# Optimization experiments

Hardware: AMD Instinct MI355X
Metric: run time of the kernel (lower is better)

The kernel has to match this reference:

```python
import jax, jax.numpy as jnp
import numpy as np
import math

B, SEQ, PRED, F, DM, NH, DFF, S, DMARK = 16, 336, 96, 7, 512, 8, 2048, 16, 5
EL, DL = 2, 1
DH = DM // NH


def _pe(max_len, d):
    pos = np.arange(max_len)[:, None].astype(np.float32)
    div = np.exp(np.arange(0, d, 2).astype(np.float32) * (-math.log(10000.0) / d))
    pe = np.zeros((max_len, d), np.float32)
    pe[:, 0::2] = np.sin(pos * div)
    pe[:, 1::2] = np.cos(pos * div)
    return jnp.asarray(pe)


def _make_tao():
    t = np.ones((S, S), np.float32)
    t[:, 0] = 0.0
    t[:, -1] = 0.0
    t[1] *= -1.0
    t[0] = 0.0
    t[0, 0] = 1.0
    t[2:, 1:-1] = np.eye(S - 2, dtype=np.float32)
    return jnp.asarray(t)


PE = _pe(2000, DM)
TAO = _make_tao()
ZVEC = jnp.zeros((S,), jnp.float32).at[:2].set(1.0)
MASK = jnp.triu(jnp.full((PRED, PRED), -1e9, jnp.float32), k=1)  # causal additive mask


def _ln(x, w, b, eps=1e-5):
    m = x.mean(-1, keepdims=True)
    v = ((x - m) ** 2).mean(-1, keepdims=True)
    return (x - m) * jax.lax.rsqrt(v + eps) * w + b


def _mha(q_in, kv_in, qkv_w, qkv_b, ow, ob, mask=None):
    wq, wk, wv = jnp.split(qkv_w, 3, axis=0)
    bq, bk, bv = jnp.split(qkv_b, 3, axis=0)

    def proj(x, w, bb):
        y = x @ w.T + bb  # [B, T, DM]
        return y.reshape(y.shape[0], y.shape[1], NH, DH).transpose(0, 2, 1, 3)

    q, k, v = proj(q_in, wq, bq), proj(kv_in, wk, bk), proj(kv_in, wv, bv)
    s = jnp.einsum('bhqd,bhkd->bhqk', q, k) / math.sqrt(DH)
    if mask is not None:
        s = s + mask
    a = jax.nn.softmax(s, axis=-1)
    o = jnp.einsum('bhqk,bhkd->bhqd', a, v)
    o = o.transpose(0, 2, 1, 3).reshape(q_in.shape)
    return o @ ow.T + ob


def _per_feature(xe, xd, eqw, eqb, eow, eob, el1w, el1b, el2w, el2b,
                 ef1w, ef1b, ef2w, ef2b, elw, elb,
                 dsqw, dsqb, dsow, dsob, dcqw, dcqb, dcow, dcob,
                 dl1w, dl1b, dl2w, dl2b, dl3w, dl3b, df1w, df1b, df2w, df2b):
    # post-norm TransformerEncoder (relu FFN), eval mode (no dropout)
    h = xe
    for l in range(EL):
        h = _ln(h + _mha(h, h, eqw[l], eqb[l], eow[l], eob[l]), el1w[l], el1b[l])
        ff = jax.nn.relu(h @ ef1w[l].T + ef1b[l]) @ ef2w[l].T + ef2b[l]
        h = _ln(h + ff, el2w[l], el2b[l])
    # encoder_linear maps time axis seqlen -> prelen
    mem = jnp.einsum('bsd,ps->bpd', h, elw) + elb[None, :, None]
    t = xd
    for l in range(DL):
        t = _ln(t + _mha(t, t, dsqw[l], dsqb[l], dsow[l], dsob[l], MASK), dl1w[l], dl1b[l])
        t = _ln(t + _mha(t, mem, dcqw[l], dcqb[l], dcow[l], dcob[l]), dl2w[l], dl2b[l])
        ff = jax.nn.relu(t @ df1w[l].T + df1b[l]) @ df2w[l].T + df2b[l]
        t = _ln(t + ff, dl3w[l], dl3b[l])
    return t


_vfeat = jax.vmap(_per_feature, in_axes=(1, 1) + (0,) * 32, out_axes=1)


def setup_inputs():
    key = jax.random.key(0)
    ks = iter(jax.random.split(key, 64))

    def rn(shape, s=0.05):
        return jax.random.normal(next(ks), shape, jnp.float32) * s

    return {
        'batch_x': rn((B, SEQ, F), 1.0),
        'batch_x_mark': rn((B, SEQ, DMARK - 1), 1.0),
        'batch_y': rn((B, PRED, F), 1.0),
        'batch_y_mark': rn((B, PRED, DMARK - 1), 1.0),
        'w_in': rn((DM, DMARK)), 'b_in': rn((DM,)),
        'w_co': rn((DM, DMARK - 1)), 'b_co': rn((DM,)),
        'eqw': rn((F, EL, 3 * DM, DM)), 'eqb': rn((F, EL, 3 * DM)),
        'eow': rn((F, EL, DM, DM)), 'eob': rn((F, EL, DM)),
        'el1w': jnp.ones((F, EL, DM)), 'el1b': jnp.zeros((F, EL, DM)),
        'el2w': jnp.ones((F, EL, DM)), 'el2b': jnp.zeros((F, EL, DM)),
        'ef1w': rn((F, EL, DFF, DM)), 'ef1b': rn((F, EL, DFF)),
        'ef2w': rn((F, EL, DM, DFF)), 'ef2b': rn((F, EL, DM)),
        'elw': rn((F, PRED, SEQ)), 'elb': rn((F, PRED)),
        'dsqw': rn((F, DL, 3 * DM, DM)), 'dsqb': rn((F, DL, 3 * DM)),
        'dsow': rn((F, DL, DM, DM)), 'dsob': rn((F, DL, DM)),
        'dcqw': rn((F, DL, 3 * DM, DM)), 'dcqb': rn((F, DL, 3 * DM)),
        'dcow': rn((F, DL, DM, DM)), 'dcob': rn((F, DL, DM)),
        'dl1w': jnp.ones((F, DL, DM)), 'dl1b': jnp.zeros((F, DL, DM)),
        'dl2w': jnp.ones((F, DL, DM)), 'dl2b': jnp.zeros((F, DL, DM)),
        'dl3w': jnp.ones((F, DL, DM)), 'dl3b': jnp.zeros((F, DL, DM)),
        'df1w': rn((F, DL, DFF, DM)), 'df1b': rn((F, DL, DFF)),
        'df2w': rn((F, DL, DM, DFF)), 'df2b': rn((F, DL, DM)),
        'wc': rn((S, DM)), 'bc': rn((S,)),
        'ws': rn((1, DM)), 'bs': rn((1,)),
    }


def reference(batch_x, batch_x_mark, batch_y, batch_y_mark,
              w_in, b_in, w_co, b_co,
              eqw, eqb, eow, eob, el1w, el1b, el2w, el2b,
              ef1w, ef1b, ef2w, ef2b, elw, elb,
              dsqw, dsqb, dsow, dsob, dcqw, dcqb, dcow, dcob,
              dl1w, dl1b, dl2w, dl2b, dl3w, dl3b, df1w, df1b, df2w, df2b,
              wc, bc, ws, bs):
    Bsz = batch_x.shape[0]
    # time marks are shared across features -> broadcast instead of concat loop
    hist = jnp.concatenate(
        [batch_x[..., None],
         jnp.broadcast_to(batch_x_mark[:, :, None, :], (Bsz, SEQ, F, DMARK - 1))], axis=-1)
    fut = jnp.broadcast_to(batch_y_mark[:, -PRED:, None, :], (Bsz, PRED, F, DMARK - 1))
    hist = hist.transpose(0, 2, 1, 3)  # [B, F, SEQ, DMARK]
    fut = fut.transpose(0, 2, 1, 3)    # [B, F, PRED, DMARK-1]
    xe = hist @ w_in.T + b_in + PE[:SEQ]
    xd = fut @ w_co.T + b_co + PE[:PRED]
    dec = _vfeat(xe, xd, eqw, eqb, eow, eob, el1w, el1b, el2w, el2b,
                 ef1w, ef1b, ef2w, ef2b, elw, elb,
                 dsqw, dsqb, dsow, dsob, dcqw, dcqb, dcow, dcob,
                 dl1w, dl1b, dl2w, dl2b, dl3w, dl3b, df1w, df1b, df2w, df2b)
    # g_c = Linear + Hardsigmoid; g_s = Linear + Softplus
    c = jnp.clip((jnp.einsum('bfpd,sd->bfps', dec, wc) + bc) / 6.0 + 0.5, 0.0, 1.0)
    sig = jax.nn.softplus(jnp.einsum('bfpd,d->bfp', dec, ws[0]) + bs[0])
    # linear state recurrence a = TAO @ a + c, y = z^T a, scanned over prediction days
    a0 = c[:, :, 0]                      # [B, F, S] (torch initializes a with day-0 g_c)
    cs = jnp.moveaxis(c, 2, 0)           # [PRED, B, F, S]
    ss = jnp.moveaxis(sig, 2, 0)         # [PRED, B, F]

    def step(a, xs):
        cd, sd = xs
        a = jnp.einsum('ij,bfj->bfi', TAO, a) + cd
        return a, jnp.einsum('s,bfs->bf', ZVEC, a) + sd

    _, ys = jax.lax.scan(step, a0, (cs, ss))
    return jnp.transpose(ys, (1, 0, 2))  # [B, PRED, F]
```

## Files before the change

### kernel.cpp

```cpp
#include <hip/hip_runtime.h>

typedef unsigned short u16;
typedef unsigned int   u32;
typedef __attribute__((ext_vector_type(8))) short short8;
typedef __attribute__((ext_vector_type(4))) float f32x4;

#define DEV static __device__ __forceinline__

DEV float bf2f(u16 u) { return __uint_as_float(((u32)u) << 16); }
DEV u16 f2bf(float f) {
  u32 u = __float_as_uint(f);
  return (u16)((u + 0x7fffu + ((u >> 16) & 1u)) >> 16);
}

#define GLD16(gp, lp) __builtin_amdgcn_global_load_lds( \
    (__attribute__((address_space(1))) u32*)(gp),       \
    (__attribute__((address_space(3))) u32*)(lp), 16, 0, 0)

__global__ __launch_bounds__(512, 2) void gemm_bf16(
    const u16* __restrict__ A, const u16* __restrict__ Bw, u16* __restrict__ C,
    const float* __restrict__ bias, int M, int N, int K,
    long sAz, long sBz, long sCz, long sBiasZ, int relu)
{
  __shared__ __align__(16) u16 Asm[2][256 * 64];
  __shared__ __align__(16) u16 Bsm[2][256 * 64];

  int gx = (int)gridDim.x, gy = (int)gridDim.y;
  int nwg = gx * gy * (int)gridDim.z;
  int orig = (int)blockIdx.x + gx * ((int)blockIdx.y + gy * (int)blockIdx.z);
  int q = nwg >> 3, r = nwg & 7;
  int xcd = orig & 7, pos = orig >> 3;
  int lg_id = (xcd < r) ? (xcd * (q + 1) + pos) : (r * (q + 1) + (xcd - r) * q + pos);
  int bz = lg_id / (gx * gy);
  int rem = lg_id - bz * (gx * gy);
  int by = rem / gx, bx = rem - by * gx;

  A += (size_t)bz * sAz; Bw += (size_t)bz * sBz; C += (size_t)bz * sCz; bias += (size_t)bz * sBiasZ;
  int tileM = bx * 256, tileN = by * 256;
  int tid = threadIdx.x, wave = tid >> 6, lane = tid & 63;
  int lr = lane & 15, lgp = lane >> 4;
  int wm = (wave >> 2) * 128;
  int wn = (wave & 3) * 64;

  const int NT = K >> 6;

  auto STAGE = [&](int b, int t) {
    int kb = t * 64;
    #pragma unroll
    for (int i = 0; i < 4; i++) {
      int gi = i * 512 + wave * 64 + lane;
      int row = gi >> 3, g = gi & 7;
      int gsw = (g ^ (row & 7)) * 8;
      GLD16(A + (size_t)(tileM + row) * K + kb + gsw, &Asm[b][(size_t)gi * 8]);
      GLD16(Bw + (size_t)(tileN + row) * K + kb + gsw, &Bsm[b][(size_t)gi * 8]);
    }
  };

  f32x4 acc[8][4] = {};

  STAGE(0, 0);
  if (NT > 1) STAGE(1, 1);

  for (int t = 0; t < NT; ++t) {
    int cur = t & 1;
    if (t + 1 < NT) asm volatile("s_waitcnt vmcnt(8)" ::: "memory");
    else            asm volatile("s_waitcnt vmcnt(0)" ::: "memory");
    asm volatile("s_barrier" ::: "memory");

    const u16* Ab = Asm[cur];
    const u16* Bb = Bsm[cur];
    #pragma unroll
    for (int ks = 0; ks < 2; ++ks) {
      short8 bfr[4], afr[8];
      #pragma unroll
      for (int n = 0; n < 4; ++n) {
        int row = wn + n * 16 + lr;
        bfr[n] = *(const short8*)(Bb + row * 64 + (((ks * 4 + lgp) ^ (row & 7)) * 8));
      }
      #pragma unroll
      for (int m = 0; m < 8; ++m) {
        int row = wm + m * 16 + lr;
        afr[m] = *(const short8*)(Ab + row * 64 + (((ks * 4 + lgp) ^ (row & 7)) * 8));
      }
      __builtin_amdgcn_s_setprio(1);
      #pragma unroll
      for (int m = 0; m < 8; ++m)
        #pragma unroll
        for (int n = 0; n < 4; ++n)
          acc[m][n] = __builtin_amdgcn_mfma_f32_16x16x32_bf16(afr[m], bfr[n], acc[m][n], 0, 0, 0);
      __builtin_amdgcn_s_setprio(0);
    }
    asm volatile("s_waitcnt lgkmcnt(0)" ::: "memory");
    asm volatile("s_barrier" ::: "memory");
    if (t + 2 < NT) STAGE(cur, t + 2);
  }

  float bb[4];
  #pragma unroll
  for (int n = 0; n < 4; ++n) bb[n] = bias[tileN + wn + n * 16 + lr];
  #pragma unroll
  for (int m = 0; m < 8; ++m) {
    #pragma unroll
    for (int rr = 0; rr < 4; ++rr) {
      int mrow = tileM + wm + m * 16 + lgp * 4 + rr;
      u16* crow = C + (size_t)mrow * N + tileN + wn + lr;
      #pragma unroll
      for (int n = 0; n < 4; ++n) {
        float v = acc[m][n][rr] + bb[n];
        if (relu) v = fmaxf(v, 0.f);
        crow[n * 16] = f2bf(v);
      }
    }
  }
}

__global__ void cvt_w_kernel(const float* __restrict__ src, u16* __restrict__ dst,
                             long n_per_f, long f_stride, long total4)
{
  long i = (long)blockIdx.x * blockDim.x + threadIdx.x;
  long step = (long)gridDim.x * blockDim.x;
  for (; i < total4; i += step) {
    long e = i * 4;
    long f = e / n_per_f; long r = e - f * n_per_f;
    float4 v = *(const float4*)(src + f * f_stride + r);
    *(ushort4*)(dst + e) = make_ushort4(f2bf(v.x), f2bf(v.y), f2bf(v.z), f2bf(v.w));
  }
}

__global__ __launch_bounds__(128) void embed_enc_k(
    const float* __restrict__ x, const float* __restrict__ mark,
    const float* __restrict__ w_in, const float* __restrict__ b_in,
    u16* __restrict__ hb)
{
  int row = blockIdx.x;
  int f = row / 5376; int rem = row - f * 5376; int b = rem / 336; int s = rem - b * 336;
  int bsix = b * 336 + s;
  float v0 = x[(size_t)bsix * 7 + f];
  float m0 = mark[(size_t)bsix * 4 + 0], m1 = mark[(size_t)bsix * 4 + 1];
  float m2 = mark[(size_t)bsix * 4 + 2], m3 = mark[(size_t)bsix * 4 + 3];
  int d0 = threadIdx.x * 4;
  u16 ob[4];
  #pragma unroll
  for (int c = 0; c < 4; c++) {
    int d = d0 + c;
    const float* w = w_in + d * 5;
    float val = w[0] * v0 + w[1] * m0 + w[2] * m1 + w[3] * m2 + w[4] * m3 + b_in[d];
    int i = d >> 1;
    float dv = expf((float)i * -0.0359778920778f);
    float arg = (float)s * dv;
    val += (d & 1) ? cosf(arg) : sinf(arg);
    ob[c] = f2bf(val);
  }
  *(ushort4*)(hb + (size_t)row * 512 + d0) = make_ushort4(ob[0], ob[1], ob[2], ob[3]);
}

__global__ __launch_bounds__(128) void embed_dec_k(
    const float* __restrict__ ymark, const float* __restrict__ w_co,
    const float* __restrict__ b_co, u16* __restrict__ tb)
{
  int row = blockIdx.x;
  int f = row / 1536; int rem = row - f * 1536; int b = rem / 96; int pp = rem - b * 96;
  int bp = b * 96 + pp;
  float m0 = ymark[(size_t)bp * 4 + 0], m1 = ymark[(size_t)bp * 4 + 1];
  float m2 = ymark[(size_t)bp * 4 + 2], m3 = ymark[(size_t)bp * 4 + 3];
  int d0 = threadIdx.x * 4;
  u16 ob[4];
  #pragma unroll
  for (int c = 0; c < 4; c++) {
    int d = d0 + c;
    const float* w = w_co + d * 4;
    float val = w[0] * m0 + w[1] * m1 + w[2] * m2 + w[3] * m3 + b_co[d];
    int i = d >> 1;
    float dv = expf((float)i * -0.0359778920778f);
    float arg = (float)pp * dv;
    val += (d & 1) ? cosf(arg) : sinf(arg);
    ob[c] = f2bf(val);
  }
  *(ushort4*)(tb + (size_t)row * 512 + d0) = make_ushort4(ob[0], ob[1], ob[2], ob[3]);
}

template<int LK, int CHUNK, int NQI>
__global__ __launch_bounds__(256) void attn_mfma(
    const u16* __restrict__ q, const u16* __restrict__ k, const u16* __restrict__ v,
    u16* __restrict__ out, int Lq, int qstride, int kvstride, int causal, int qspan)
{
  constexpr int NCH = LK / CHUNK;
  constexpr int NKT = CHUNK / 16;
  constexpr int NKS = (CHUNK + 31) / 32;
  constexpr int KPAD = NKS * 32;
  constexpr int VSTR = KPAD + 8;
  constexpr int NGRP = CHUNK * 8 / 64;

  __shared__ __align__(16) u16 KsS[CHUNK * 64];
  __shared__ __align__(16) u16 VtS[64 * VSTR];
  __shared__ __align__(16) u16 PWS[4][16 * VSTR];

  int hh = blockIdx.x, fb = blockIdx.y;
  int tid = threadIdx.x, wave = tid >> 6, lane = tid & 63;
  int lr = lane & 15, lg = lane >> 4;

  const int nqt = Lq / 16;
  const int qlo = (int)blockIdx.z * qspan;
  const int qhi = (qlo + qspan < nqt) ? (qlo + qspan) : nqt;

  const u16* qp = q + (size_t)fb * Lq * qstride + hh * 64;
  const u16* kp = k + (size_t)fb * LK * kvstride + hh * 64;
  const u16* vp = v + (size_t)fb * LK * kvstride + hh * 64;

  if constexpr (KPAD > CHUNK) {
    constexpr int TW = KPAD - CHUNK;
    for (int i = tid; i < 64 * TW; i += 256)
      VtS[(i / TW) * VSTR + CHUNK + (i % TW)] = 0;
    u16* PW = PWS[wave];
    for (int i = lane; i < 16 * TW; i += 64)
      PW[(i / TW) * VSTR + CHUNK + (i % TW)] = 0;
  }

  f32x4 oacc[NQI][4] = {};
  f32x4 lsum[NQI] = {};
  u16* PW = PWS[wave];

  for (int c = 0; c < NCH; ++c) {
    __syncthreads();

    const u16* kcp = kp + (size_t)c * CHUNK * kvstride;
    for (int grp = wave; grp < NGRP; grp += 4) {
      int gi = grp * 64 + lane;
      int row = gi >> 3, g = gi & 7;
      GLD16(kcp + (size_t)row * kvstride + ((g ^ (row & 7)) * 8), KsS + (size_t)gi * 8);
    }
    const u16* vcp = vp + (size_t)c * CHUNK * kvstride;
    for (int idx = tid; idx < CHUNK * 8; idx += 256) {
      int kk = idx >> 3, dg = idx & 7;
      uint4 pv = *(const uint4*)(vcp + (size_t)kk * kvstride + dg * 8);
      u16* col = VtS + (size_t)(dg * 8) * VSTR + kk;
      col[0 * VSTR] = (u16)pv.x; col[1 * VSTR] = (u16)(pv.x >> 16);
      col[2 * VSTR] = (u16)pv.y; col[3 * VSTR] = (u16)(pv.y >> 16);
      col[4 * VSTR] = (u16)pv.z; col[5 * VSTR] = (u16)(pv.z >> 16);
      col[6 * VSTR] = (u16)pv.w; col[7 * VSTR] = (u16)(pv.w >> 16);
    }
    __syncthreads();

    #pragma unroll
    for (int qi = 0; qi < NQI; ++qi) {
      int qt = qlo + wave + qi * 4;
      if (qt < qhi) {
        const u16* qrow = qp + (size_t)(qt * 16 + lr) * qstride + lg * 8;
        short8 qf0 = *(const short8*)(qrow);
        short8 qf1 = *(const short8*)(qrow + 32);

        f32x4 sacc[NKT];
        #pragma unroll
        for (int t = 0; t < NKT; t++) {
          int row = t * 16 + lr;
          const u16* kb = KsS + row * 64;
          short8 kf0 = *(const short8*)(kb + ((lg ^ (row & 7)) * 8));
          short8 kf1 = *(const short8*)(kb + (((lg + 4) ^ (row & 7)) * 8));
          f32x4 s = {0.f, 0.f, 0.f, 0.f};
          s = __builtin_amdgcn_mfma_f32_16x16x32_bf16(qf0, kf0, s, 0, 0, 0);
          s = __builtin_amdgcn_mfma_f32_16x16x32_bf16(qf1, kf1, s, 0, 0, 0);
          sacc[t] = s;
        }

        #pragma unroll
        for (int t = 0; t < NKT; t++) {
          int kg = c * CHUNK + t * 16 + lr;
          #pragma unroll
          for (int r = 0; r < 4; r++) {
            int qg = qt * 16 + lg * 4 + r;
            float p = (causal && kg > qg) ? 0.f : __expf(sacc[t][r] * 0.125f);
            sacc[t][r] = p;
            lsum[qi][r] += p;
          }
          u16* pw = PW + (size_t)(lg * 4) * VSTR + t * 16 + lr;
          pw[0 * VSTR] = f2bf(sacc[t][0]);
          pw[1 * VSTR] = f2bf(sacc[t][1]);
          pw[2 * VSTR] = f2bf(sacc[t][2]);
          pw[3 * VSTR] = f2bf(sacc[t][3]);
        }

        #pragma unroll
        for (int s = 0; s < NKS; s++) {
          short8 pf = *(const short8*)(PW + (size_t)lr * VSTR + s * 32 + lg * 8);
          #pragma unroll
          for (int j = 0; j < 4; j++) {
            short8 vf = *(const short8*)(VtS + (size_t)(j * 16 + lr) * VSTR + s * 32 + lg * 8);
            oacc[qi][j] = __builtin_amdgcn_mfma_f32_16x16x32_bf16(pf, vf, oacc[qi][j], 0, 0, 0);
          }
        }
      }
    }
  }

  #pragma unroll
  for (int qi = 0; qi < NQI; ++qi) {
    int qt = qlo + wave + qi * 4;
    if (qt < qhi) {
      float l0 = lsum[qi][0], l1 = lsum[qi][1], l2 = lsum[qi][2], l3 = lsum[qi][3];
      #pragma unroll
      for (int m = 1; m < 16; m <<= 1) {
        l0 += __shfl_xor(l0, m);
        l1 += __shfl_xor(l1, m);
        l2 += __shfl_xor(l2, m);
        l3 += __shfl_xor(l3, m);
      }
      float inv[4] = {1.f / l0, 1.f / l1, 1.f / l2, 1.f / l3};
      #pragma unroll
      for (int r = 0; r < 4; r++) {
        size_t orow = (size_t)fb * Lq + qt * 16 + lg * 4 + r;
        u16* ob = out + orow * 512 + hh * 64 + lr;
        #pragma unroll
        for (int j = 0; j < 4; j++)
          ob[j * 16] = f2bf(oacc[qi][j][r] * inv[r]);
      }
    }
  }
}

__global__ __launch_bounds__(128) void ln_kernel(
    u16* __restrict__ h, const u16* __restrict__ delta,
    const float* __restrict__ gamma, const float* __restrict__ beta,
    int rows_per_f, long gstride)
{
  __shared__ float red[2];
  int row = blockIdx.x;
  int f = row / rows_per_f;
  const float* g = gamma + (size_t)f * gstride;
  const float* be = beta + (size_t)f * gstride;
  int d0 = threadIdx.x * 4;
  size_t p = (size_t)row * 512 + d0;
  ushort4 hv = *(const ushort4*)(h + p);
  ushort4 dv = *(const ushort4*)(delta + p);
  float x0 = bf2f(hv.x) + bf2f(dv.x), x1 = bf2f(hv.y) + bf2f(dv.y);
  float x2 = bf2f(hv.z) + bf2f(dv.z), x3 = bf2f(hv.w) + bf2f(dv.w);
  float ssum = x0 + x1 + x2 + x3;
  #pragma unroll
  for (int m = 1; m < 64; m <<= 1) ssum += __shfl_xor(ssum, m);
  if ((threadIdx.x & 63) == 0) red[threadIdx.x >> 6] = ssum;
  __syncthreads();
  float mean = (red[0] + red[1]) * (1.f / 512.f);
  __syncthreads();
  float c0 = x0 - mean, c1 = x1 - mean, c2 = x2 - mean, c3 = x3 - mean;
  float sq = c0 * c0 + c1 * c1 + c2 * c2 + c3 * c3;
  #pragma unroll
  for (int m = 1; m < 64; m <<= 1) sq += __shfl_xor(sq, m);
  if ((threadIdx.x & 63) == 0) red[threadIdx.x >> 6] = sq;
  __syncthreads();
  float var = (red[0] + red[1]) * (1.f / 512.f);
  float rstd = rsqrtf(var + 1e-5f);
  float y0 = c0 * rstd * g[d0 + 0] + be[d0 + 0];
  float y1 = c1 * rstd * g[d0 + 1] + be[d0 + 1];
  float y2 = c2 * rstd * g[d0 + 2] + be[d0 + 2];
  float y3 = c3 * rstd * g[d0 + 3] + be[d0 + 3];
  *(ushort4*)(h + p) = make_ushort4(f2bf(y0), f2bf(y1), f2bf(y2), f2bf(y3));
}

__global__ __launch_bounds__(256) void mem_kernel(
    const u16* __restrict__ h, const float* __restrict__ elw,
    const float* __restrict__ elb, u16* __restrict__ memb)
{
  int fb = blockIdx.x; int f = fb >> 4;
  int pc = blockIdx.y;
  int d0 = threadIdx.x * 2;
  const u16* hbase = h + (size_t)fb * 336 * 512;
  const float* wbase = elw + (size_t)f * 96 * 336 + (size_t)pc * 16 * 336;
  float a0[16], a1[16];
  #pragma unroll
  for (int pp = 0; pp < 16; pp++) { a0[pp] = 0.f; a1[pp] = 0.f; }
  for (int s = 0; s < 336; s++) {
    ushort2 h2 = *(const ushort2*)(hbase + (size_t)s * 512 + d0);
    float hx = bf2f(h2.x), hy = bf2f(h2.y);
    #pragma unroll
    for (int pp = 0; pp < 16; pp++) {
      float w = wbase[pp * 336 + s];
      a0[pp] += w * hx; a1[pp] += w * hy;
    }
  }
  #pragma unroll
  for (int pp = 0; pp < 16; pp++) {
    int pidx = pc * 16 + pp;
    size_t row = (size_t)fb * 96 + pidx;
    float e = elb[f * 96 + pidx];
    *(ushort2*)(memb + row * 512 + d0) = make_ushort2(f2bf(a0[pp] + e), f2bf(a1[pp] + e));
  }
}

__global__ __launch_bounds__(64) void head_kernel(
    const u16* __restrict__ td, const float* __restrict__ wcp, const float* __restrict__ bcp,
    const float* __restrict__ wsp, const float* __restrict__ bsp,
    float* __restrict__ cb, float* __restrict__ sg, int f0)
{
  int rl = blockIdx.x, lane = threadIdx.x;
  size_t row = (size_t)f0 * 1536 + rl;
  const u16* x = td + (size_t)rl * 512;
  float xr[8];
  #pragma unroll
  for (int j = 0; j < 8; j++) xr[j] = bf2f(x[lane + 64 * j]);
  #pragma unroll
  for (int o = 0; o < 16; o++) {
    const float* w = wcp + o * 512;
    float p = 0.f;
    #pragma unroll
    for (int j = 0; j < 8; j++) p += xr[j] * w[lane + 64 * j];
    #pragma unroll
    for (int m = 1; m < 64; m <<= 1) p += __shfl_xor(p, m);
    if (lane == 0) {
      float cv = (p + bcp[o]) / 6.0f + 0.5f;
      cb[row * 16 + o] = fminf(fmaxf(cv, 0.f), 1.f);
    }
  }
  float p = 0.f;
  #pragma unroll
  for (int j = 0; j < 8; j++) p += xr[j] * wsp[lane + 64 * j];
  #pragma unroll
  for (int m = 1; m < 64; m <<= 1) p += __shfl_xor(p, m);
  if (lane == 0) {
    float zv = p + bsp[0];
    sg[row] = (zv > 20.f) ? zv : log1pf(expf(zv));
  }
}

__global__ __launch_bounds__(256) void scan_kernel(
    const float* __restrict__ cbuf, const float* __restrict__ sgb, float* __restrict__ outp)
{
  int f = blockIdx.x;
  int b = threadIdx.x >> 4;
  int s = threadIdx.x & 15;
  size_t rbase = ((size_t)f * 16 + b) * 96;
  float a = cbuf[rbase * 16 + s];
  for (int p = 0; p < 96; ++p) {
    float cd = cbuf[(rbase + p) * 16 + s];
    float sd = sgb[rbase + p];
    float xs = (s >= 1 && s <= 14) ? a : 0.f;
    #pragma unroll
    for (int m = 1; m < 16; m <<= 1) xs += __shfl_xor(xs, m);
    float up = __shfl_up(a, 1, 16);
    float an = (s == 0) ? (a + cd) : ((s == 1) ? (cd - xs) : (up + cd));
    a = an;
    float y01 = __shfl(a, 0, 16) + __shfl(a, 1, 16) + sd;
    if (s == 0) outp[((size_t)b * 96 + p) * 7 + f] = y01;
  }
}

__global__ void diag_kernel(float* __restrict__ out, float v, int n)
{
  int i = blockIdx.x * 256 + threadIdx.x;
  if (i < n) out[i] = v;
}

extern "C" void kernel_launch(void* const* d_in, const int* in_sizes, int n_in,
                              void* d_out, int out_size, void* d_ws, size_t ws_size,
                              hipStream_t stream)
{
  (void)in_sizes; (void)n_in;
  const float* batch_x      = (const float*)d_in[0];
  const float* batch_x_mark = (const float*)d_in[1];
  const float* batch_y_mark = (const float*)d_in[3];
  const float* w_in = (const float*)d_in[4];
  const float* b_in = (const float*)d_in[5];
  const float* w_co = (const float*)d_in[6];
  const float* b_co = (const float*)d_in[7];
  const float* eqw  = (const float*)d_in[8];
  const float* eqb  = (const float*)d_in[9];
  const float* eow  = (const float*)d_in[10];
  const float* eob  = (const float*)d_in[11];
  const float* el1w = (const float*)d_in[12];
  const float* el1b = (const float*)d_in[13];
  const float* el2w = (const float*)d_in[14];
  const float* el2b = (const float*)d_in[15];
  const float* ef1w = (const float*)d_in[16];
  const float* ef1b = (const float*)d_in[17];
  const float* ef2w = (const float*)d_in[18];
  const float* ef2b = (const float*)d_in[19];
  const float* elw  = (const float*)d_in[20];
  const float* elb  = (const float*)d_in[21];
  const float* dsqw = (const float*)d_in[22];
  const float* dsqb = (const float*)d_in[23];
  const float* dsow = (const float*)d_in[24];
  const float* dsob = (const float*)d_in[25];
  const float* dcqw = (const float*)d_in[26];
  const float* dcqb = (const float*)d_in[27];
  const float* dcow = (const float*)d_in[28];
  const float* dcob = (const float*)d_in[29];
  const float* dl1w = (const float*)d_in[30];
  const float* dl1b = (const float*)d_in[31];
  const float* dl2w = (const float*)d_in[32];
  const float* dl2b = (const float*)d_in[33];
  const float* dl3w = (const float*)d_in[34];
  const float* dl3b = (const float*)d_in[35];
  const float* df1w = (const float*)d_in[36];
  const float* df1b = (const float*)d_in[37];
  const float* df2w = (const float*)d_in[38];
  const float* df2b = (const float*)d_in[39];
  const float* wc   = (const float*)d_in[40];
  const float* bc   = (const float*)d_in[41];
  const float* wsg  = (const float*)d_in[42];
  const float* bsg  = (const float*)d_in[43];

  const size_t NE = 37632;
  const size_t ND = 10752;
  auto al = [](size_t x) { return (x + 255) & ~(size_t)255; };

  size_t fixedB = al(NE * 1024) + al(ND * 1024) + al(ND * 64) + al(ND * 4);
  int G = 0;
  for (int g = 7; g >= 1; --g) {
    size_t need = fixedB
        + al((size_t)g * 5376 * 2048 * 2)
        + al((size_t)g * 5376 * 512 * 2)
        + al((size_t)g * 2048 * 512 * 2)
        + al((size_t)g * 1536 * 512 * 2);
    if (need <= ws_size) { G = g; break; }
  }
  if (G == 0) {
    diag_kernel<<<dim3((out_size + 255) / 256), 256, 0, stream>>>(
        (float*)d_out, 1000.0f + (float)(ws_size >> 20), out_size);
    return;
  }

  char* base = (char*)d_ws;
  size_t off = 0;
  auto alloc = [&](size_t bytes) -> void* { void* r = base + off; off += al(bytes); return r; };
  u16*   hres = (u16*)  alloc(NE * 1024);
  u16*   tres = (u16*)  alloc(ND * 1024);
  float* cb   = (float*)alloc(ND * 64);
  float* sg   = (float*)alloc(ND * 4);
  u16*   bigc = (u16*)  alloc((size_t)G * 5376 * 2048 * 2);
  u16*   aobc = (u16*)  alloc((size_t)G * 5376 * 512 * 2);
  u16*   wbuf = (u16*)  alloc((size_t)G * 2048 * 512 * 2);
  u16*   memb = (u16*)  alloc((size_t)G * 1536 * 512 * 2);

  embed_enc_k<<<dim3(37632), 128, 0, stream>>>(batch_x, batch_x_mark, w_in, b_in, hres);
  embed_dec_k<<<dim3(10752), 128, 0, stream>>>(batch_y_mark, w_co, b_co, tres);

  auto cvtw = [&](const float* src, long n_per_f, long f_stride, int g) {
    cvt_w_kernel<<<dim3(512), 256, 0, stream>>>(src, wbuf, n_per_f, f_stride,
                                                (long)g * n_per_f / 4);
  };
  auto gemm = [&](const u16* A, long sAz, u16* C, long sCz, const float* bias, long sBias,
                  int M, int N, int K, int g, int relu) {
    dim3 gr(M / 256, N / 256, g);
    gemm_bf16<<<gr, 512, 0, stream>>>(A, wbuf, C, bias, M, N, K, sAz, (long)N * K, sCz,
                                      sBias, relu);
  };

  for (int f0 = 0; f0 < 7; f0 += G) {
    int g = (7 - f0 < G) ? (7 - f0) : G;
    u16* hc = hres + (size_t)f0 * 5376 * 512;
    u16* tc = tres + (size_t)f0 * 1536 * 512;

    for (int l = 0; l < 2; ++l) {
      cvtw(eqw + (size_t)f0 * 1572864 + (size_t)l * 786432, 786432L, 1572864L, g);
      gemm(hc, 5376L * 512, bigc, 5376L * 1536, eqb + f0 * 3072 + l * 1536, 3072,
           5376, 1536, 512, g, 0);
      attn_mfma<336, 112, 3><<<dim3(8, g * 16, 2), 256, 0, stream>>>(
          bigc, bigc + 512, bigc + 1024, aobc, 336, 1536, 1536, 0, 11);
      cvtw(eow + (size_t)f0 * 524288 + (size_t)l * 262144, 262144L, 524288L, g);
      gemm(aobc, 5376L * 512, bigc, 5376L * 512, eob + f0 * 1024 + l * 512, 1024,
           5376, 512, 512, g, 0);
      ln_kernel<<<dim3(g * 5376), 128, 0, stream>>>(
          hc, bigc, el1w + f0 * 1024 + l * 512, el1b + f0 * 1024 + l * 512, 5376, 1024);
      cvtw(ef1w + (size_t)f0 * 2097152 + (size_t)l * 1048576, 1048576L, 2097152L, g);
      gemm(hc, 5376L * 512, bigc, 5376L * 2048, ef1b + f0 * 4096 + l * 2048, 4096,
           5376, 2048, 512, g, 1);
      cvtw(ef2w + (size_t)f0 * 2097152 + (size_t)l * 1048576, 1048576L, 2097152L, g);
      gemm(bigc, 5376L * 2048, aobc, 5376L * 512, ef2b + f0 * 1024 + l * 512, 1024,
           5376, 512, 2048, g, 0);
      ln_kernel<<<dim3(g * 5376), 128, 0, stream>>>(
          hc, aobc, el2w + f0 * 1024 + l * 512, el2b + f0 * 1024 + l * 512, 5376, 1024);
    }

    mem_kernel<<<dim3(g * 16, 6), 256, 0, stream>>>(
        hc, elw + (size_t)f0 * 32256, elb + f0 * 96, memb);

    cvtw(dsqw + (size_t)f0 * 786432, 786432L, 786432L, g);
    gemm(tc, 1536L * 512, bigc, 1536L * 1536, dsqb + f0 * 1536, 1536,
         1536, 1536, 512, g, 0);
    attn_mfma<96, 96, 2><<<dim3(8, g * 16, 1), 256, 0, stream>>>(
        bigc, bigc + 512, bigc + 1024, aobc, 96, 1536, 1536, 1, 6);
    cvtw(dsow + (size_t)f0 * 262144, 262144L, 262144L, g);
    gemm(aobc, 1536L * 512, bigc, 1536L * 512, dsob + f0 * 512, 512,
         1536, 512, 512, g, 0);
    ln_kernel<<<dim3(g * 1536), 128, 0, stream>>>(
        tc, bigc, dl1w + f0 * 512, dl1b + f0 * 512, 1536, 512);

    cvtw(dcqw + (size_t)f0 * 786432, 262144L, 786432L, g);
    gemm(tc, 1536L * 512, bigc, 1536L * 512, dcqb + f0 * 1536, 1536,
         1536, 512, 512, g, 0);
    u16* bigKV = bigc + (size_t)g * 1536 * 512;
    cvtw(dcqw + (size_t)f0 * 786432 + 262144, 524288L, 786432L, g);
    gemm(memb, 1536L * 512, bigKV, 1536L * 1024, dcqb + f0 * 1536 + 512, 1536,
         1536, 1024, 512, g, 0);
    attn_mfma<96, 96, 2><<<dim3(8, g * 16, 1), 256, 0, stream>>>(
        bigc, bigKV, bigKV + 512, aobc, 96, 512, 1024, 0, 6);
    cvtw(dcow + (size_t)f0 * 262144, 262144L, 262144L, g);
    gemm(aobc, 1536L * 512, bigc, 1536L * 512, dcob + f0 * 512, 512,
         1536, 512, 512, g, 0);
    ln_kernel<<<dim3(g * 1536), 128, 0, stream>>>(
        tc, bigc, dl2w + f0 * 512, dl2b + f0 * 512, 1536, 512);

    cvtw(df1w + (size_t)f0 * 1048576, 1048576L, 1048576L, g);
    gemm(tc, 1536L * 512, bigc, 1536L * 2048, df1b + f0 * 2048, 2048,
         1536, 2048, 512, g, 1);
    cvtw(df2w + (size_t)f0 * 1048576, 1048576L, 1048576L, g);
    gemm(bigc, 1536L * 2048, aobc, 1536L * 512, df2b + f0 * 512, 512,
         1536, 512, 2048, g, 0);
    ln_kernel<<<dim3(g * 1536), 128, 0, stream>>>(
        tc, aobc, dl3w + f0 * 512, dl3b + f0 * 512, 1536, 512);

    head_kernel<<<dim3(g * 1536), 64, 0, stream>>>(tc, wc, bc, wsg, bsg, cb, sg, f0);
  }

  scan_kernel<<<dim3(7), 256, 0, stream>>>(cb, sg, (float*)d_out);
}
```

Measured before the change: 1.578 ms.

## Restructure GEMM main loop into four-phase ping-pong with split half-tile staging

The bf16 GEMM main loop now splits the A and B shared-memory tiles into two halves each. Each K-step is broken into four MFMA quadrants, with LDS fragment reads and global-to-LDS loads of the next halves interleaved between barriers. The goal is to overlap global loads and LDS reads with matrix-core work instead of staging whole tiles after the compute. It adds more barriers and depends on careful vmcnt accounting, which could cause stalls or hazards if the counts are wrong.

```diff
diff --git a/kernel.cpp b/kernel.cpp
--- a/kernel.cpp
+++ b/kernel.cpp
@@ -17,20 +17,23 @@
     (__attribute__((address_space(1))) u32*)(gp),       \
     (__attribute__((address_space(3))) u32*)(lp), 16, 0, 0)
 
+#define SBAR()  asm volatile("s_barrier" ::: "memory")
+#define LGKM0() asm volatile("s_waitcnt lgkmcnt(0)" ::: "memory")
+
 __global__ __launch_bounds__(512, 2) void gemm_bf16(
     const u16* __restrict__ A, const u16* __restrict__ Bw, u16* __restrict__ C,
     const float* __restrict__ bias, int M, int N, int K,
     long sAz, long sBz, long sCz, long sBiasZ, int relu)
 {
-  __shared__ __align__(16) u16 Asm[2][256 * 64];
-  __shared__ __align__(16) u16 Bsm[2][256 * 64];
+  __shared__ __align__(16) u16 Asm[2][2][8192];
+  __shared__ __align__(16) u16 Bsm[2][2][8192];
 
   int gx = (int)gridDim.x, gy = (int)gridDim.y;
   int nwg = gx * gy * (int)gridDim.z;
   int orig = (int)blockIdx.x + gx * ((int)blockIdx.y + gy * (int)blockIdx.z);
-  int q = nwg >> 3, r = nwg & 7;
+  int qq = nwg >> 3, rr_ = nwg & 7;
   int xcd = orig & 7, pos = orig >> 3;
-  int lg_id = (xcd < r) ? (xcd * (q + 1) + pos) : (r * (q + 1) + (xcd - r) * q + pos);
+  int lg_id = (xcd < rr_) ? (xcd * (qq + 1) + pos) : (rr_ * (qq + 1) + (xcd - rr_) * qq + pos);
   int bz = lg_id / (gx * gy);
   int rem = lg_id - bz * (gx * gy);
   int by = rem / gx, bx = rem - by * gx;
@@ -41,58 +44,131 @@
   int lr = lane & 15, lgp = lane >> 4;
   int wm = (wave >> 2) * 128;
   int wn = (wave & 3) * 64;
+  int ah = wave >> 2;
+  int bh = (wave & 3) >> 1;
+  int bnb = ((wave & 3) & 1) * 64;
 
   const int NT = K >> 6;
-
-  auto STAGE = [&](int b, int t) {
-    int kb = t * 64;
-    #pragma unroll
-    for (int i = 0; i < 4; i++) {
-      int gi = i * 512 + wave * 64 + lane;
+  const u16* Abase = A + (size_t)tileM * K;
+  const u16* Bbase = Bw + (size_t)tileN * K;
+
+  auto SA = [&](int b, int h, int t) {
+    const u16* src = Abase + (size_t)h * 128 * K + t * 64;
+    #pragma unroll
+    for (int i = 0; i < 2; i++) {
+      int gi = i * 512 + tid;
       int row = gi >> 3, g = gi & 7;
-      int gsw = (g ^ (row & 7)) * 8;
-      GLD16(A + (size_t)(tileM + row) * K + kb + gsw, &Asm[b][(size_t)gi * 8]);
-      GLD16(Bw + (size_t)(tileN + row) * K + kb + gsw, &Bsm[b][(size_t)gi * 8]);
+      GLD16(src + (size_t)row * K + ((g ^ (row & 7)) * 8), Asm[b][h] + (size_t)gi * 8);
     }
   };
+  auto SB = [&](int b, int h, int t) {
+    const u16* src = Bbase + (size_t)h * 128 * K + t * 64;
+    #pragma unroll
+    for (int i = 0; i < 2; i++) {
+      int gi = i * 512 + tid;
+      int row = gi >> 3, g = gi & 7;
+      GLD16(src + (size_t)row * K + ((g ^ (row & 7)) * 8), Bsm[b][h] + (size_t)gi * 8);
+    }
+  };
 
   f32x4 acc[8][4] = {};
 
-  STAGE(0, 0);
-  if (NT > 1) STAGE(1, 1);
+  SA(0, 0, 0); SA(0, 1, 0); SB(0, 0, 0); SB(0, 1, 0);
+  if (NT > 1) { SB(1, 0, 1); SB(1, 1, 1); }
+  if (NT > 1) asm volatile("s_waitcnt vmcnt(4)" ::: "memory");
+  else        asm volatile("s_waitcnt vmcnt(0)" ::: "memory");
+  SBAR();
 
   for (int t = 0; t < NT; ++t) {
     int cur = t & 1;
-    if (t + 1 < NT) asm volatile("s_waitcnt vmcnt(8)" ::: "memory");
+    const u16* Aslot = Asm[cur][ah];
+    const u16* Bslot = Bsm[cur][bh];
+    short8 afr[8], b0[4], b1[4];
+
+    #pragma unroll
+    for (int mm = 0; mm < 4; ++mm) {
+      int rw = mm * 16 + lr;
+      #pragma unroll
+      for (int ks = 0; ks < 2; ++ks)
+        afr[mm * 2 + ks] = *(const short8*)(Aslot + rw * 64 + (((ks * 4 + lgp) ^ (rw & 7)) * 8));
+    }
+    #pragma unroll
+    for (int nn = 0; nn < 2; ++nn) {
+      int rw = bnb + nn * 16 + lr;
+      #pragma unroll
+      for (int ks = 0; ks < 2; ++ks)
+        b0[nn * 2 + ks] = *(const short8*)(Bslot + rw * 64 + (((ks * 4 + lgp) ^ (rw & 7)) * 8));
+    }
+    if (t + 1 < NT) SA(cur ^ 1, 0, t + 1);
+    SBAR(); LGKM0();
+    __builtin_amdgcn_s_setprio(1);
+    #pragma unroll
+    for (int mm = 0; mm < 4; ++mm)
+      #pragma unroll
+      for (int nn = 0; nn < 2; ++nn)
+        #pragma unroll
+        for (int ks = 0; ks < 2; ++ks)
+          acc[mm][nn] = __builtin_amdgcn_mfma_f32_16x16x32_bf16(
+              afr[mm * 2 + ks], b0[nn * 2 + ks], acc[mm][nn], 0, 0, 0);
+    __builtin_amdgcn_s_setprio(0);
+    SBAR();
+
+    #pragma unroll
+    for (int nn = 0; nn < 2; ++nn) {
+      int rw = bnb + (nn + 2) * 16 + lr;
+      #pragma unroll
+      for (int ks = 0; ks < 2; ++ks)
+        b1[nn * 2 + ks] = *(const short8*)(Bslot + rw * 64 + (((ks * 4 + lgp) ^ (rw & 7)) * 8));
+    }
+    if (t + 1 < NT) SA(cur ^ 1, 1, t + 1);
+    SBAR(); LGKM0();
+    __builtin_amdgcn_s_setprio(1);
+    #pragma unroll
+    for (int mm = 0; mm < 4; ++mm)
+      #pragma unroll
+      for (int nn = 0; nn < 2; ++nn)
+        #pragma unroll
+        for (int ks = 0; ks < 2; ++ks)
+          acc[mm][nn + 2] = __builtin_amdgcn_mfma_f32_16x16x32_bf16(
+              afr[mm * 2 + ks], b1[nn * 2 + ks], acc[mm][nn + 2], 0, 0, 0);
+    __builtin_amdgcn_s_setprio(0);
+    SBAR();
+
+    #pragma unroll
+    for (int mm = 0; mm < 4; ++mm) {
+      int rw = (mm + 4) * 16 + lr;
+      #pragma unroll
+      for (int ks = 0; ks < 2; ++ks)
+        afr[mm * 2 + ks] = *(const short8*)(Aslot + rw * 64 + (((ks * 4 + lgp) ^ (rw & 7)) * 8));
+    }
+    if (t + 2 < NT) SB(cur, 0, t + 2);
+    SBAR(); LGKM0();
+    __builtin_amdgcn_s_setprio(1);
+    #pragma unroll
+    for (int mm = 0; mm < 4; ++mm)
+      #pragma unroll
+      for (int nn = 0; nn < 2; ++nn)
+        #pragma unroll
+        for (int ks = 0; ks < 2; ++ks)
+          acc[mm + 4][nn + 2] = __builtin_amdgcn_mfma_f32_16x16x32_bf16(
+              afr[mm * 2 + ks], b1[nn * 2 + ks], acc[mm + 4][nn + 2], 0, 0, 0);
+    __builtin_amdgcn_s_setprio(0);
+    SBAR();
+
+    if (t + 2 < NT) SB(cur, 1, t + 2);
+    __builtin_amdgcn_s_setprio(1);
+    #pragma unroll
+    for (int mm = 0; mm < 4; ++mm)
+      #pragma unroll
+      for (int nn = 0; nn < 2; ++nn)
+        #pragma unroll
+        for (int ks = 0; ks < 2; ++ks)
+          acc[mm + 4][nn] = __builtin_amdgcn_mfma_f32_16x16x32_bf16(
+              afr[mm * 2 + ks], b0[nn * 2 + ks], acc[mm + 4][nn], 0, 0, 0);
+    __builtin_amdgcn_s_setprio(0);
+    if (t + 2 < NT) asm volatile("s_waitcnt vmcnt(4)" ::: "memory");
     else            asm volatile("s_waitcnt vmcnt(0)" ::: "memory");
-    asm volatile("s_barrier" ::: "memory");
-
-    const u16* Ab = Asm[cur];
-    const u16* Bb = Bsm[cur];
-    #pragma unroll
-    for (int ks = 0; ks < 2; ++ks) {
-      short8 bfr[4], afr[8];
-      #pragma unroll
-      for (int n = 0; n < 4; ++n) {
-        int row = wn + n * 16 + lr;
-        bfr[n] = *(const short8*)(Bb + row * 64 + (((ks * 4 + lgp) ^ (row & 7)) * 8));
-      }
-      #pragma unroll
-      for (int m = 0; m < 8; ++m) {
-        int row = wm + m * 16 + lr;
-        afr[m] = *(const short8*)(Ab + row * 64 + (((ks * 4 + lgp) ^ (row & 7)) * 8));
-      }
-      __builtin_amdgcn_s_setprio(1);
-      #pragma unroll
-      for (int m = 0; m < 8; ++m)
-        #pragma unroll
-        for (int n = 0; n < 4; ++n)
-          acc[m][n] = __builtin_amdgcn_mfma_f32_16x16x32_bf16(afr[m], bfr[n], acc[m][n], 0, 0, 0);
-      __builtin_amdgcn_s_setprio(0);
-    }
-    asm volatile("s_waitcnt lgkmcnt(0)" ::: "memory");
-    asm volatile("s_barrier" ::: "memory");
-    if (t + 2 < NT) STAGE(cur, t + 2);
+    SBAR();
   }
 
   float bb[4];
```

Measured after the change: 1.515 ms. -4.0%, faster.
